# Kernel optimization log

Hardware: AMD Instinct MI355X
Metric: run time of the kernel (lower is better)

The kernel has to match this reference:

```python
import jax, jax.numpy as jnp
import numpy as np

B, D, S = 16, 512, 1500   # batch, input_size, seq_len
E, K, L = 8, 1024, 8      # embedding_size, num_embeddings, num_layers
TAU = 1.0
EPS = 1e-12               # F.normalize default eps


def setup_inputs() -> dict:
    key = jax.random.key(0)
    ks = jax.random.split(key, 5)
    x = jax.random.normal(ks[0], (B, D, S), dtype=jnp.float32)
    # weight-norm parametrized 1x1 conv params (v direction, g magnitude, bias)
    in_v = jax.random.normal(ks[1], (L, E, D), dtype=jnp.float32) * 0.05
    in_g = jnp.ones((L, E), dtype=jnp.float32)
    in_b = jnp.zeros((L, E), dtype=jnp.float32)
    out_v = jax.random.normal(ks[2], (L, D, E), dtype=jnp.float32) * 0.05
    out_g = jnp.ones((L, D), dtype=jnp.float32)
    out_b = jnp.zeros((L, D), dtype=jnp.float32)
    codebook = jax.random.normal(ks[3], (L, K, E), dtype=jnp.float32)
    return dict(x=x, in_v=in_v, in_g=in_g, in_b=in_b,
                out_v=out_v, out_g=out_g, out_b=out_b, codebook=codebook)


def _wn(v, g):
    # torch weight_norm (dim=0): w = g * v / ||v|| with norm over all dims except out-channel
    n = jnp.sqrt(jnp.sum(v * v, axis=1, keepdims=True))
    return g[:, None] * v / n


def _l2norm(x):
    # F.normalize(p=2, eps=1e-12)
    n = jnp.linalg.norm(x, axis=-1, keepdims=True)
    return x / jnp.maximum(n, EPS)


def _vq_layer(xr, iv, ig, ib, ov, og, ob, cb):
    Wi = _wn(iv, ig)                                              # [E, D]
    x_proj = jnp.einsum('ed,bds->bes', Wi, xr) + ib[:, None]      # [B, E, S]
    xf = x_proj.transpose(0, 2, 1).reshape(B * S, E)              # [B*S, E]
    xn = _l2norm(xf)
    cn = _l2norm(cb)                                              # [K, E]
    dist = (jnp.sum(xn * xn, axis=1, keepdims=True)
            - 2.0 * (xn @ cn.T)
            + jnp.sum(cn * cn, axis=1)[None, :])                  # [B*S, K]
    logits = -dist / TAU
    idxs = jnp.argmax(-dist, axis=1).reshape(B, S)                # [B, S]
    xq = cb[idxs].transpose(0, 2, 1)                              # [B, E, S] (un-normalized codebook)
    commit = jnp.mean((x_proj - jax.lax.stop_gradient(xq)) ** 2, axis=(1, 2))  # per-batch
    cbloss = jnp.mean((xq - jax.lax.stop_gradient(x_proj)) ** 2, axis=(1, 2))
    xq_st = x_proj + jax.lax.stop_gradient(xq - x_proj)           # straight-through
    Wo = _wn(ov, og)                                              # [D, E]
    xq_out = jnp.einsum('de,bes->bds', Wo, xq_st) + ob[:, None]   # [B, D, S]
    return xq_out, logits, idxs, commit, cbloss


def reference(x, in_v, in_g, in_b, out_v, out_g, out_b, codebook):
    # eval mode: all layers active, mask all-ones => masked mean == plain batch mean
    xq_sum = jnp.zeros_like(x)
    xr = x
    idxs_l, logits_l = [], []
    commit = jnp.float32(0.0)
    cbl = jnp.float32(0.0)
    for i in range(L):
        xq, lg, ix, cl, bl = _vq_layer(xr, in_v[i], in_g[i], in_b[i],
                                       out_v[i], out_g[i], out_b[i], codebook[i])
        xq_sum = xq_sum + xq
        xr = xr - xq
        commit = commit + jnp.mean(cl)
        cbl = cbl + jnp.mean(bl)
        idxs_l.append(ix)
        logits_l.append(lg)
    x_idxs = jnp.stack(idxs_l, axis=1)     # [B, L, S]
    x_logits = jnp.stack(logits_l, axis=1) # [B*S, L, K]
    return xq_sum, x_idxs, x_logits, commit, cbl
```

## Files before the change

kernel.cpp:

```cpp
#include <hip/hip_runtime.h>

constexpr int Lx = 8;
constexpr int Bx = 16;
constexpr int Dx = 512;
constexpr int Sx = 1500;
constexpr int Ex = 8;
constexpr int Kx = 1024;
constexpr int BS = Bx * Sx;
#define EPSF 1e-12f

__global__ __launch_bounds__(64) void k_wn_in(const float* __restrict__ v,
                                              const float* __restrict__ g,
                                              float* __restrict__ WiT) {
    int row = blockIdx.x;
    int l = row >> 3, e = row & 7;
    int lane = threadIdx.x;
    const float* vr = v + row * Dx;
    float s = 0.f;
    for (int j = lane; j < Dx; j += 64) { float t = vr[j]; s += t * t; }
    for (int off = 32; off; off >>= 1) s += __shfl_down(s, off);
    s = __shfl(s, 0);
    float scale = g[row] / sqrtf(s);
    for (int j = lane; j < Dx; j += 64)
        WiT[((size_t)l * Dx + j) * Ex + e] = vr[j] * scale;
}

__global__ __launch_bounds__(256) void k_wn_out_cb(const float* __restrict__ ov,
                                                   const float* __restrict__ og,
                                                   const float* __restrict__ cb,
                                                   float* __restrict__ Wo,
                                                   float* __restrict__ cn,
                                                   float* __restrict__ cc,
                                                   double* __restrict__ acc) {
    int r = blockIdx.x * blockDim.x + threadIdx.x;
    if (r == 0) *acc = 0.0;
    if (r < Lx * Dx) {
        const float* vr = ov + r * Ex;
        float s = 0.f;
        #pragma unroll
        for (int e = 0; e < Ex; e++) s += vr[e] * vr[e];
        float sc = og[r] / sqrtf(s);
        #pragma unroll
        for (int e = 0; e < Ex; e++) Wo[r * Ex + e] = vr[e] * sc;
    } else {
        int q = r - Lx * Dx;
        if (q < Lx * Kx) {
            const float* vr = cb + q * Ex;
            float s = 0.f;
            #pragma unroll
            for (int e = 0; e < Ex; e++) s += vr[e] * vr[e];
            float n = fmaxf(sqrtf(s), EPSF);
            float s2 = 0.f, qv[Ex];
            #pragma unroll
            for (int e = 0; e < Ex; e++) { qv[e] = vr[e] / n; s2 += qv[e] * qv[e]; }
            #pragma unroll
            for (int e = 0; e < Ex; e++) cn[q * Ex + e] = qv[e];
            cc[q] = s2;
        }
    }
}

__global__ __launch_bounds__(256, 3) void k_mega(const float* __restrict__ x,
                                                 const float* __restrict__ WiT,
                                                 const float* __restrict__ ibias,
                                                 const float* __restrict__ Wo,
                                                 const float* __restrict__ obias,
                                                 const float* __restrict__ cb,
                                                 const float* __restrict__ cn,
                                                 const float* __restrict__ cc,
                                                 float* __restrict__ out0,
                                                 float* __restrict__ oidx,
                                                 float* __restrict__ logits,
                                                 double* __restrict__ acc) {
    __shared__ float4 cnA[Kx];
    __shared__ float4 cnB[Kx];
    __shared__ float  ccs[Kx];
    __shared__ float  red[8 * Ex * 32];
    __shared__ float  xprojs[Ex * 32];
    __shared__ float  xqs[Ex * 32];
    __shared__ float  bred[4];

    const int t = threadIdx.x;
    const int col = t & 31;
    const int g = t >> 5;
    const int wave = t >> 6, lane = t & 63;
    const int c = blockIdx.x * 32 + col;
    const int b = c / Sx;
    const int s = c - b * Sx;
    const float* xcol = x + (size_t)b * Dx * Sx + s;

    float xr[64];
    #pragma unroll
    for (int i = 0; i < 64; i++) xr[i] = xcol[(size_t)(g * 64 + i) * Sx];

    float lossp = 0.f;

    for (int l = 0; l < Lx; l++) {
        const float4* cn4 = (const float4*)(cn + (size_t)l * Kx * Ex);
        const float4* cc4 = (const float4*)(cc + l * Kx);
        float4 ra[4], rb[4], rc;
        #pragma unroll
        for (int q = 0; q < 4; q++) {
            ra[q] = cn4[(t + 256 * q) * 2];
            rb[q] = cn4[(t + 256 * q) * 2 + 1];
        }
        rc = cc4[t];

        const float4* wt = (const float4*)(WiT + (size_t)l * Dx * Ex);
        float pacc[8] = {0, 0, 0, 0, 0, 0, 0, 0};
        #pragma unroll
        for (int i = 0; i < 64; i++) {
            int d = g * 64 + i;
            float4 w0 = wt[d * 2 + 0];
            float4 w1 = wt[d * 2 + 1];
            float v = xr[i];
            pacc[0] += w0.x * v; pacc[1] += w0.y * v;
            pacc[2] += w0.z * v; pacc[3] += w0.w * v;
            pacc[4] += w1.x * v; pacc[5] += w1.y * v;
            pacc[6] += w1.z * v; pacc[7] += w1.w * v;
        }
        #pragma unroll
        for (int e = 0; e < 8; e++) red[(g * 8 + e) * 32 + col] = pacc[e];

        #pragma unroll
        for (int q = 0; q < 4; q++) {
            cnA[t + 256 * q] = ra[q];
            cnB[t + 256 * q] = rb[q];
        }
        *(float4*)&ccs[t * 4] = rc;
        __syncthreads();

        {
            float sum = 0.f;
            #pragma unroll
            for (int gg = 0; gg < 8; gg++) sum += red[(gg * 8 + g) * 32 + col];
            xprojs[g * 32 + col] = sum + ibias[l * Ex + g];
        }
        __syncthreads();

        for (int pass = 0; pass < 2; pass++) {
            const int colbase = wave * 8 + pass * 4;
            float xn2[4][8];
            float xc[4], best[4];
            int bk[4];
            float* lrow[4];
            #pragma unroll
            for (int c4 = 0; c4 < 4; c4++) {
                int mycol = colbase + c4;
                int mc = blockIdx.x * 32 + mycol;
                float xp[8]; float xx2 = 0.f;
                #pragma unroll
                for (int e = 0; e < 8; e++) {
                    xp[e] = xprojs[e * 32 + mycol];
                    xx2 += xp[e] * xp[e];
                }
                float nrm = fmaxf(sqrtf(xx2), EPSF);
                float xx = 0.f;
                #pragma unroll
                for (int e = 0; e < 8; e++) {
                    float xnv = xp[e] / nrm;
                    xx += xnv * xnv;
                    xn2[c4][e] = 2.f * xnv;
                }
                xc[c4] = xx;
                best[c4] = -3.0e38f;
                bk[c4] = 0;
                lrow[c4] = logits + ((size_t)mc * Lx + l) * Kx;
            }
            #pragma unroll 2
            for (int j = 0; j < 16; j++) {
                int k = j * 64 + lane;
                float4 a  = cnA[k];
                float4 b4 = cnB[k];
                float  cv = ccs[k];
                #pragma unroll
                for (int c4 = 0; c4 < 4; c4++) {
                    float dot2 = xn2[c4][0] * a.x  + xn2[c4][1] * a.y +
                                 xn2[c4][2] * a.z  + xn2[c4][3] * a.w +
                                 xn2[c4][4] * b4.x + xn2[c4][5] * b4.y +
                                 xn2[c4][6] * b4.z + xn2[c4][7] * b4.w;
                    float lg = -(xc[c4] - dot2 + cv);
                    lrow[c4][k] = lg;
                    if (lg > best[c4]) { best[c4] = lg; bk[c4] = k; }
                }
            }
            #pragma unroll
            for (int c4 = 0; c4 < 4; c4++) {
                float bv = best[c4]; int bi = bk[c4];
                for (int off = 32; off; off >>= 1) {
                    float ov = __shfl_xor(bv, off);
                    int   oi = __shfl_xor(bi, off);
                    if (ov > bv || (ov == bv && oi < bi)) { bv = ov; bi = oi; }
                }
                int mycol = colbase + c4;
                int mc = blockIdx.x * 32 + mycol;
                int mb = mc / Sx, ms = mc - mb * Sx;
                if (lane == 0) oidx[((size_t)mb * Lx + l) * Sx + ms] = (float)bi;
                if (lane < 8) {
                    float q = cb[((size_t)l * Kx + bi) * Ex + lane];
                    xqs[lane * 32 + mycol] = q;
                    float dl = xprojs[lane * 32 + mycol] - q;
                    lossp += dl * dl;
                }
            }
        }
        __syncthreads();

        float xq[8];
        #pragma unroll
        for (int e = 0; e < 8; e++) xq[e] = xqs[e * 32 + col];
        const float4* wo4 = (const float4*)(Wo + (size_t)l * Dx * Ex);
        const float* obl = obias + l * Dx;
        #pragma unroll
        for (int i = 0; i < 64; i++) {
            int d = g * 64 + i;
            float4 w0 = wo4[d * 2 + 0];
            float4 w1 = wo4[d * 2 + 1];
            float dsum = w0.x * xq[0] + w0.y * xq[1] + w0.z * xq[2] + w0.w * xq[3] +
                         w1.x * xq[4] + w1.y * xq[5] + w1.z * xq[6] + w1.w * xq[7] +
                         obl[d];
            xr[i] -= dsum;
        }
    }

    float* ocol = out0 + (size_t)b * Dx * Sx + s;
    #pragma unroll
    for (int i = 0; i < 64; i++) {
        float xv = xcol[(size_t)(g * 64 + i) * Sx];
        ocol[(size_t)(g * 64 + i) * Sx] = xv - xr[i];
    }

    for (int off = 32; off; off >>= 1) lossp += __shfl_down(lossp, off);
    if (lane == 0) bred[wave] = lossp;
    __syncthreads();
    if (t == 0)
        atomicAdd(acc, (double)(bred[0] + bred[1] + bred[2] + bred[3]));
}

__global__ void k_scalar(const double* __restrict__ acc,
                         float* __restrict__ commit, float* __restrict__ cbl) {
    if (threadIdx.x == 0) {
        float v = (float)(*acc / (double)((size_t)Bx * Ex * Sx));
        *commit = v;
        *cbl = v;
    }
}

extern "C" void kernel_launch(void* const* d_in, const int* in_sizes, int n_in,
                              void* d_out, int out_size, void* d_ws, size_t ws_size,
                              hipStream_t stream) {
    const float* x     = (const float*)d_in[0];
    const float* in_v  = (const float*)d_in[1];
    const float* in_g  = (const float*)d_in[2];
    const float* in_b  = (const float*)d_in[3];
    const float* out_v = (const float*)d_in[4];
    const float* out_g = (const float*)d_in[5];
    const float* out_b = (const float*)d_in[6];
    const float* cb    = (const float*)d_in[7];

    float* out = (float*)d_out;
    float* out0     = out;
    float* oidx     = out + 12288000;
    float* ologits  = out + 12480000;
    float* ocommit  = out + 209088000;
    float* ocbl     = out + 209088001;

    char* w = (char*)d_ws;
    float*  WiT   = (float*)(w);
    float*  Wo    = (float*)(w + 131072);
    float*  cn    = (float*)(w + 262144);
    float*  cc    = (float*)(w + 524288);
    double* acc   = (double*)(w + 557056);

    k_wn_in<<<Lx * Ex, 64, 0, stream>>>(in_v, in_g, WiT);
    k_wn_out_cb<<<(Lx * Dx + Lx * Kx) / 256, 256, 0, stream>>>(out_v, out_g, cb,
                                                               Wo, cn, cc, acc);
    k_mega<<<BS / 32, 256, 0, stream>>>(x, WiT, in_b, Wo, out_b, cb, cn, cc,
                                        out0, oidx, ologits, acc);
    k_scalar<<<1, 64, 0, stream>>>(acc, ocommit, ocbl);
}
```

Measured before the change: 623.1 us.

## Load codebook to LDS via direct global_load_lds and alias reduction buffer

Replaces the register-staged codebook and norm loads with direct global-to-LDS 16-byte loads issued after the projection reduction. The reduction scratch is aliased onto the codebook LDS buffer, which cuts LDS use and allows occupancy to rise from 3 to 4 blocks per CU. Barriers become explicit lgkmcnt waits plus s_barrier. The trade-off is that the codebook load no longer overlaps the projection compute, so it is now exposed, and the higher occupancy may force register spilling of the 64-element xr array.

```diff
diff --git a/kernel.cpp b/kernel.cpp
--- a/kernel.cpp
+++ b/kernel.cpp
@@ -8,6 +8,18 @@
 constexpr int Kx = 1024;
 constexpr int BS = Bx * Sx;
 #define EPSF 1e-12f
+
+__device__ __forceinline__ void lds_barrier() {
+    asm volatile("s_waitcnt lgkmcnt(0)" ::: "memory");
+    __builtin_amdgcn_s_barrier();
+    asm volatile("" ::: "memory");
+}
+
+__device__ __forceinline__ void gload_lds16(const void* g, void* l) {
+    __builtin_amdgcn_global_load_lds(
+        (const __attribute__((address_space(1))) void*)g,
+        (__attribute__((address_space(3))) void*)l, 16, 0, 0);
+}
 
 __global__ __launch_bounds__(64) void k_wn_in(const float* __restrict__ v,
                                               const float* __restrict__ g,
@@ -60,7 +72,7 @@
     }
 }
 
-__global__ __launch_bounds__(256, 3) void k_mega(const float* __restrict__ x,
+__global__ __launch_bounds__(256, 4) void k_mega(const float* __restrict__ x,
                                                  const float* __restrict__ WiT,
                                                  const float* __restrict__ ibias,
                                                  const float* __restrict__ Wo,
@@ -75,10 +87,10 @@
     __shared__ float4 cnA[Kx];
     __shared__ float4 cnB[Kx];
     __shared__ float  ccs[Kx];
-    __shared__ float  red[8 * Ex * 32];
     __shared__ float  xprojs[Ex * 32];
     __shared__ float  xqs[Ex * 32];
     __shared__ float  bred[4];
+    float* red = (float*)cnA;
 
     const int t = threadIdx.x;
     const int col = t & 31;
@@ -96,16 +108,6 @@
     float lossp = 0.f;
 
     for (int l = 0; l < Lx; l++) {
-        const float4* cn4 = (const float4*)(cn + (size_t)l * Kx * Ex);
-        const float4* cc4 = (const float4*)(cc + l * Kx);
-        float4 ra[4], rb[4], rc;
-        #pragma unroll
-        for (int q = 0; q < 4; q++) {
-            ra[q] = cn4[(t + 256 * q) * 2];
-            rb[q] = cn4[(t + 256 * q) * 2 + 1];
-        }
-        rc = cc4[t];
-
         const float4* wt = (const float4*)(WiT + (size_t)l * Dx * Ex);
         float pacc[8] = {0, 0, 0, 0, 0, 0, 0, 0};
         #pragma unroll
@@ -121,14 +123,7 @@
         }
         #pragma unroll
         for (int e = 0; e < 8; e++) red[(g * 8 + e) * 32 + col] = pacc[e];
-
-        #pragma unroll
-        for (int q = 0; q < 4; q++) {
-            cnA[t + 256 * q] = ra[q];
-            cnB[t + 256 * q] = rb[q];
-        }
-        *(float4*)&ccs[t * 4] = rc;
-        __syncthreads();
+        lds_barrier();
 
         {
             float sum = 0.f;
@@ -136,7 +131,21 @@
             for (int gg = 0; gg < 8; gg++) sum += red[(gg * 8 + g) * 32 + col];
             xprojs[g * 32 + col] = sum + ibias[l * Ex + g];
         }
-        __syncthreads();
+        lds_barrier();
+
+        {
+            const char* cs = (const char*)(cn + (size_t)l * Kx * Ex);
+            const char* zs = (const char*)(cc + (size_t)l * Kx);
+            #pragma unroll
+            for (int q = 0; q < 4; q++) {
+                const char* srcp = cs + (size_t)(wave * 256 + q * 64 + lane) * 32;
+                gload_lds16(srcp,      (char*)cnA + wave * 4096 + q * 1024);
+                gload_lds16(srcp + 16, (char*)cnB + wave * 4096 + q * 1024);
+            }
+            gload_lds16(zs + (size_t)(wave * 64 + lane) * 16, (char*)ccs + wave * 1024);
+            asm volatile("s_waitcnt vmcnt(0)" ::: "memory");
+        }
+        lds_barrier();
 
         for (int pass = 0; pass < 2; pass++) {
             const int colbase = wave * 8 + pass * 4;
@@ -204,7 +213,7 @@
                 }
             }
         }
-        __syncthreads();
+        lds_barrier();
 
         float xq[8];
         #pragma unroll
@@ -232,7 +241,7 @@
 
     for (int off = 32; off; off >>= 1) lossp += __shfl_down(lossp, off);
     if (lane == 0) bred[wave] = lossp;
-    __syncthreads();
+    lds_barrier();
     if (t == 0)
         atomicAdd(acc, (double)(bred[0] + bred[1] + bred[2] + bred[3]));
 }
```

Measured after the change: 732.1 us. 1.18x slower.

## Remap threads so each wave owns its columns, replacing LDS reductions with shuffles

Applied to the files above, without the earlier changes.

Thread-to-data mapping changes so each wave owns 8 columns split across 8 D-slabs in its lanes. The input projection reduction, normalization, index broadcast and codebook gather then happen in-wave via shuffles instead of shared-memory staging. This drops the red/xprojs/xqs LDS arrays and two block barriers per layer, and uses a lighter custom barrier. Occupancy hint rises from 3 to 4 blocks per CU. The cost is that x loads become less coalesced (8 contiguous columns per slab instead of 32), and the tighter register budget may cause spills.

```diff
diff --git a/kernel.cpp b/kernel.cpp
--- a/kernel.cpp
+++ b/kernel.cpp
@@ -8,6 +8,12 @@
 constexpr int Kx = 1024;
 constexpr int BS = Bx * Sx;
 #define EPSF 1e-12f
+
+__device__ __forceinline__ void lds_barrier() {
+    asm volatile("s_waitcnt lgkmcnt(0)" ::: "memory");
+    __builtin_amdgcn_s_barrier();
+    asm volatile("" ::: "memory");
+}
 
 __global__ __launch_bounds__(64) void k_wn_in(const float* __restrict__ v,
                                               const float* __restrict__ g,
@@ -60,7 +66,7 @@
     }
 }
 
-__global__ __launch_bounds__(256, 3) void k_mega(const float* __restrict__ x,
+__global__ __launch_bounds__(256, 4) void k_mega(const float* __restrict__ x,
                                                  const float* __restrict__ WiT,
                                                  const float* __restrict__ ibias,
                                                  const float* __restrict__ Wo,
@@ -75,29 +81,26 @@
     __shared__ float4 cnA[Kx];
     __shared__ float4 cnB[Kx];
     __shared__ float  ccs[Kx];
-    __shared__ float  red[8 * Ex * 32];
-    __shared__ float  xprojs[Ex * 32];
-    __shared__ float  xqs[Ex * 32];
     __shared__ float  bred[4];
 
     const int t = threadIdx.x;
-    const int col = t & 31;
-    const int g = t >> 5;
     const int wave = t >> 6, lane = t & 63;
-    const int c = blockIdx.x * 32 + col;
+    const int colL = lane & 7;
+    const int slab = lane >> 3;
+    const int c = blockIdx.x * 32 + wave * 8 + colL;
     const int b = c / Sx;
     const int s = c - b * Sx;
     const float* xcol = x + (size_t)b * Dx * Sx + s;
 
     float xr[64];
     #pragma unroll
-    for (int i = 0; i < 64; i++) xr[i] = xcol[(size_t)(g * 64 + i) * Sx];
+    for (int i = 0; i < 64; i++) xr[i] = xcol[(size_t)(slab * 64 + i) * Sx];
 
     float lossp = 0.f;
 
     for (int l = 0; l < Lx; l++) {
         const float4* cn4 = (const float4*)(cn + (size_t)l * Kx * Ex);
-        const float4* cc4 = (const float4*)(cc + l * Kx);
+        const float4* cc4 = (const float4*)(cc + (size_t)l * Kx);
         float4 ra[4], rb[4], rc;
         #pragma unroll
         for (int q = 0; q < 4; q++) {
@@ -110,7 +113,7 @@
         float pacc[8] = {0, 0, 0, 0, 0, 0, 0, 0};
         #pragma unroll
         for (int i = 0; i < 64; i++) {
-            int d = g * 64 + i;
+            int d = slab * 64 + i;
             float4 w0 = wt[d * 2 + 0];
             float4 w1 = wt[d * 2 + 1];
             float v = xr[i];
@@ -120,51 +123,51 @@
             pacc[6] += w1.z * v; pacc[7] += w1.w * v;
         }
         #pragma unroll
-        for (int e = 0; e < 8; e++) red[(g * 8 + e) * 32 + col] = pacc[e];
-
+        for (int off = 8; off <= 32; off <<= 1) {
+            #pragma unroll
+            for (int e = 0; e < 8; e++) pacc[e] += __shfl_xor(pacc[e], off);
+        }
+        float xproj_my[8];
+        #pragma unroll
+        for (int e = 0; e < 8; e++) xproj_my[e] = pacc[e] + ibias[l * Ex + e];
+
+        float xx2 = 0.f;
+        #pragma unroll
+        for (int e = 0; e < 8; e++) xx2 += xproj_my[e] * xproj_my[e];
+        float nrm = fmaxf(sqrtf(xx2), EPSF);
+        float xx_my = 0.f, xn2_my[8];
+        #pragma unroll
+        for (int e = 0; e < 8; e++) {
+            float xnv = xproj_my[e] / nrm;
+            xx_my += xnv * xnv;
+            xn2_my[e] = 2.f * xnv;
+        }
+
+        lds_barrier();
         #pragma unroll
         for (int q = 0; q < 4; q++) {
             cnA[t + 256 * q] = ra[q];
             cnB[t + 256 * q] = rb[q];
         }
-        *(float4*)&ccs[t * 4] = rc;
-        __syncthreads();
-
-        {
-            float sum = 0.f;
-            #pragma unroll
-            for (int gg = 0; gg < 8; gg++) sum += red[(gg * 8 + g) * 32 + col];
-            xprojs[g * 32 + col] = sum + ibias[l * Ex + g];
-        }
-        __syncthreads();
-
+        ((float4*)ccs)[t] = rc;
+        lds_barrier();
+
+        int bi_mine = 0;
+        #pragma unroll
         for (int pass = 0; pass < 2; pass++) {
-            const int colbase = wave * 8 + pass * 4;
             float xn2[4][8];
             float xc[4], best[4];
             int bk[4];
             float* lrow[4];
             #pragma unroll
             for (int c4 = 0; c4 < 4; c4++) {
-                int mycol = colbase + c4;
-                int mc = blockIdx.x * 32 + mycol;
-                float xp[8]; float xx2 = 0.f;
+                const int src = pass * 4 + c4;
                 #pragma unroll
-                for (int e = 0; e < 8; e++) {
-                    xp[e] = xprojs[e * 32 + mycol];
-                    xx2 += xp[e] * xp[e];
-                }
-                float nrm = fmaxf(sqrtf(xx2), EPSF);
-                float xx = 0.f;
-                #pragma unroll
-                for (int e = 0; e < 8; e++) {
-                    float xnv = xp[e] / nrm;
-                    xx += xnv * xnv;
-                    xn2[c4][e] = 2.f * xnv;
-                }
-                xc[c4] = xx;
+                for (int e = 0; e < 8; e++) xn2[c4][e] = __shfl(xn2_my[e], src);
+                xc[c4] = __shfl(xx_my, src);
                 best[c4] = -3.0e38f;
                 bk[c4] = 0;
+                int mc = blockIdx.x * 32 + wave * 8 + src;
                 lrow[c4] = logits + ((size_t)mc * Lx + l) * Kx;
             }
             #pragma unroll 2
@@ -192,28 +195,33 @@
                     int   oi = __shfl_xor(bi, off);
                     if (ov > bv || (ov == bv && oi < bi)) { bv = ov; bi = oi; }
                 }
-                int mycol = colbase + c4;
-                int mc = blockIdx.x * 32 + mycol;
-                int mb = mc / Sx, ms = mc - mb * Sx;
-                if (lane == 0) oidx[((size_t)mb * Lx + l) * Sx + ms] = (float)bi;
-                if (lane < 8) {
-                    float q = cb[((size_t)l * Kx + bi) * Ex + lane];
-                    xqs[lane * 32 + mycol] = q;
-                    float dl = xprojs[lane * 32 + mycol] - q;
-                    lossp += dl * dl;
+                const int src = pass * 4 + c4;
+                if (colL == src) bi_mine = bi;
+                if (lane == 0) {
+                    int mc = blockIdx.x * 32 + wave * 8 + src;
+                    int mb = mc / Sx, ms = mc - mb * Sx;
+                    oidx[((size_t)mb * Lx + l) * Sx + ms] = (float)bi;
                 }
             }
         }
-        __syncthreads();
-
-        float xq[8];
-        #pragma unroll
-        for (int e = 0; e < 8; e++) xq[e] = xqs[e * 32 + col];
+
+        const float4* cbr = (const float4*)(cb + ((size_t)l * Kx + bi_mine) * Ex);
+        float4 q0 = cbr[0], q1 = cbr[1];
+        float xq[8] = {q0.x, q0.y, q0.z, q0.w, q1.x, q1.y, q1.z, q1.w};
+
+        if (slab == 0) {
+            #pragma unroll
+            for (int e = 0; e < 8; e++) {
+                float dl = xproj_my[e] - xq[e];
+                lossp += dl * dl;
+            }
+        }
+
         const float4* wo4 = (const float4*)(Wo + (size_t)l * Dx * Ex);
         const float* obl = obias + l * Dx;
         #pragma unroll
         for (int i = 0; i < 64; i++) {
-            int d = g * 64 + i;
+            int d = slab * 64 + i;
             float4 w0 = wo4[d * 2 + 0];
             float4 w1 = wo4[d * 2 + 1];
             float dsum = w0.x * xq[0] + w0.y * xq[1] + w0.z * xq[2] + w0.w * xq[3] +
@@ -226,8 +234,8 @@
     float* ocol = out0 + (size_t)b * Dx * Sx + s;
     #pragma unroll
     for (int i = 0; i < 64; i++) {
-        float xv = xcol[(size_t)(g * 64 + i) * Sx];
-        ocol[(size_t)(g * 64 + i) * Sx] = xv - xr[i];
+        float xv = xcol[(size_t)(slab * 64 + i) * Sx];
+        ocol[(size_t)(slab * 64 + i) * Sx] = xv - xr[i];
     }
 
     for (int off = 32; off; off >>= 1) lossp += __shfl_down(lossp, off);
```

Result: slower. 704.8 us (+13.1%).
